# Kernel optimization log

Measured on AMD Instinct MI355X. Metric: run time of the kernel, lower is better.

## Reference

```python
import jax, jax.numpy as jnp
import numpy as np

DIM = 768
NUM_HEADS = 12
HEAD_DIM = DIM // NUM_HEADS
ROPE_BASE = 10000.0


def _rope_angles(height, width, head_dim, base):
    # 2D RoPE: first half of head_dim rotates with the row (y) position,
    # second half with the column (x) position.
    half = head_dim // 2            # dims per spatial axis
    quarter = half // 2             # rotation pair count per axis
    inv_freq = 1.0 / (base ** (jnp.arange(0, half, 2, dtype=jnp.float32) / half))  # [quarter]
    ys = jnp.arange(height, dtype=jnp.float32)
    xs = jnp.arange(width, dtype=jnp.float32)
    ang_y = ys[:, None] * inv_freq  # [H, quarter]
    ang_x = xs[:, None] * inv_freq  # [W, quarter]
    ay = jnp.broadcast_to(ang_y[:, None, :], (height, width, quarter)).reshape(height * width, quarter)
    ax = jnp.broadcast_to(ang_x[None, :, :], (height, width, quarter)).reshape(height * width, quarter)
    return ay, ax


def _rotate(t, ang):
    # t: [B, nh, N, half]; ang: [N, quarter]. Interleaved pair rotation.
    c, s = jnp.cos(ang), jnp.sin(ang)
    t1, t2 = t[..., 0::2], t[..., 1::2]
    r1 = t1 * c - t2 * s
    r2 = t1 * s + t2 * c
    return jnp.stack([r1, r2], axis=-1).reshape(t.shape)


def apply_2d_rope(t, height, width, base):
    # t: [B, nh, N, head_dim]
    hd = t.shape[-1]
    half = hd // 2
    ay, ax = _rope_angles(height, width, hd, base)
    return jnp.concatenate([_rotate(t[..., :half], ay), _rotate(t[..., half:], ax)], axis=-1)


def setup_inputs() -> dict:
    key = jax.random.key(0)
    ks = jax.random.split(key, 5)
    B, N = 16, 32 * 32
    x = jax.random.normal(ks[0], (B, N, DIM), dtype=jnp.float32)
    qkv_w = jax.random.normal(ks[1], (3 * DIM, DIM), dtype=jnp.float32) * (1.0 / np.sqrt(DIM))
    qkv_b = jnp.zeros((3 * DIM,), dtype=jnp.float32)
    proj_w = jax.random.normal(ks[2], (DIM, DIM), dtype=jnp.float32) * (1.0 / np.sqrt(DIM))
    proj_b = jnp.zeros((DIM,), dtype=jnp.float32)
    return {"x": x, "qkv_w": qkv_w, "qkv_b": qkv_b, "proj_w": proj_w,
            "proj_b": proj_b, "height": 32, "width": 32}


def reference(x, qkv_w, qkv_b, proj_w, proj_b, height, width):
    B, N, C = x.shape
    scale = 1.0 / np.sqrt(HEAD_DIM)
    qkv = x @ qkv_w.T + qkv_b                      # [B, N, 3*C]
    qkv = qkv.reshape(B, N, 3, NUM_HEADS, HEAD_DIM).transpose(2, 0, 3, 1, 4)
    q, k, v = qkv[0], qkv[1], qkv[2]               # [B, nh, N, hd]
    q = apply_2d_rope(q, height, width, ROPE_BASE)
    k = apply_2d_rope(k, height, width, ROPE_BASE)
    attn = jnp.einsum('bhnd,bhmd->bhnm', q, k) * scale
    attn = jax.nn.softmax(attn, axis=-1)
    out = jnp.einsum('bhnm,bhmd->bhnd', attn, v)   # [B, nh, N, hd]
    out = out.transpose(0, 2, 1, 3).reshape(B, N, C)
    return out @ proj_w.T + proj_b
```

## Files before the change

### kernel.cpp

```cpp
#include <hip/hip_runtime.h>
#include <hip/hip_bf16.h>

typedef _Float16 f16;
typedef _Float16 half8 __attribute__((ext_vector_type(8)));
typedef _Float16 half4 __attribute__((ext_vector_type(4)));
typedef float f32x4 __attribute__((ext_vector_type(4)));
typedef unsigned short u16;
typedef unsigned int u32;

#define AS_GLOBAL __attribute__((address_space(1)))
#define AS_LDS    __attribute__((address_space(3)))

static __device__ __forceinline__ f32x4 mfma_k32(half8 a, half8 b, f32x4 c) {
  return __builtin_amdgcn_mfma_f32_16x16x32_f16(a, b, c, 0, 0, 0);
}

static __device__ __forceinline__ void glds16(const void* g, void* l) {
  __builtin_amdgcn_global_load_lds((const AS_GLOBAL u32*)(unsigned long long)g,
                                   (AS_LDS u32*)l, 16, 0, 0);
}

__global__ __launch_bounds__(256) void cvt_kernel(const float* __restrict__ src,
                                                  f16* __restrict__ dst, int n) {
  long i = ((long)blockIdx.x * 256 + threadIdx.x) * 8;
  if (i + 8 <= n) {
    const float4 a = *(const float4*)(src + i);
    const float4 b = *(const float4*)(src + i + 4);
    union { uint4 v; f16 h[8]; } o;
    o.h[0] = (f16)a.x; o.h[1] = (f16)a.y; o.h[2] = (f16)a.z; o.h[3] = (f16)a.w;
    o.h[4] = (f16)b.x; o.h[5] = (f16)b.y; o.h[6] = (f16)b.z; o.h[7] = (f16)b.w;
    *(uint4*)(dst + i) = o.v;
  }
}

static __device__ __forceinline__ void gemm128p(const f16* __restrict__ A, const f16* __restrict__ B,
                                                const int K, const long m0, const long n0,
                                                f16* As, f16* Bs, f32x4 acc[4][4]) {
  const int tid = threadIdx.x;
  const int lane = tid & 63, w = tid >> 6;
  const int l15 = lane & 15, qd = lane >> 4;
  const int wr = w >> 1, wc = w & 1;
  const int srow = w * 16 + (lane >> 2);
  const int sg   = ((lane & 3) ^ ((lane >> 3) & 3)) * 8;
  const f16* gA0 = A + (m0 + srow) * (long)K + sg;
  const f16* gA1 = gA0 + 64 * (long)K;
  const f16* gB0 = B + (n0 + srow) * (long)K + sg;
  const f16* gB1 = gB0 + 64 * (long)K;
  f16* lA = As + w * 512;
  f16* lB = Bs + w * 512;
  const int rg   = (qd ^ ((l15 >> 1) & 3)) * 8;
  const int arow = (wr * 64 + l15) * 32;
  const int brow = (wc * 64 + l15) * 32;
  const int nT = K >> 5;

#define STAGE(t) { const long ko = (long)(t) * 32;                         \
    f16* dA = lA + ((t) % 3) * 4096; f16* dB = lB + ((t) % 3) * 4096;      \
    glds16(gA0 + ko, dA); glds16(gA1 + ko, dA + 2048);                     \
    glds16(gB0 + ko, dB); glds16(gB1 + ko, dB + 2048); }

  STAGE(0); STAGE(1);
  asm volatile("s_waitcnt vmcnt(4)" ::: "memory");
  __builtin_amdgcn_sched_barrier(0);
  __builtin_amdgcn_s_barrier();
  __builtin_amdgcn_sched_barrier(0);
#pragma unroll
  for (int t = 0; t < nT; ++t) {
    if (t + 2 < nT) STAGE(t + 2);
    const f16* cA = As + (t % 3) * 4096;
    const f16* cB = Bs + (t % 3) * 4096;
    half8 a0[2], a1[2], b0[2], b1[2];
    a0[0] = *(const half8*)(cA + arow + rg);
    a0[1] = *(const half8*)(cA + arow + 512 + rg);
    b0[0] = *(const half8*)(cB + brow + rg);
    b0[1] = *(const half8*)(cB + brow + 512 + rg);
    __builtin_amdgcn_s_setprio(1);
    acc[0][0] = mfma_k32(a0[0], b0[0], acc[0][0]);
    acc[0][1] = mfma_k32(a0[0], b0[1], acc[0][1]);
    acc[1][0] = mfma_k32(a0[1], b0[0], acc[1][0]);
    acc[1][1] = mfma_k32(a0[1], b0[1], acc[1][1]);
    __builtin_amdgcn_s_setprio(0);
    b1[0] = *(const half8*)(cB + brow + 1024 + rg);
    b1[1] = *(const half8*)(cB + brow + 1536 + rg);
    __builtin_amdgcn_s_setprio(1);
    acc[0][2] = mfma_k32(a0[0], b1[0], acc[0][2]);
    acc[0][3] = mfma_k32(a0[0], b1[1], acc[0][3]);
    acc[1][2] = mfma_k32(a0[1], b1[0], acc[1][2]);
    acc[1][3] = mfma_k32(a0[1], b1[1], acc[1][3]);
    __builtin_amdgcn_s_setprio(0);
    a1[0] = *(const half8*)(cA + arow + 1024 + rg);
    a1[1] = *(const half8*)(cA + arow + 1536 + rg);
    __builtin_amdgcn_s_setprio(1);
    acc[2][2] = mfma_k32(a1[0], b1[0], acc[2][2]);
    acc[2][3] = mfma_k32(a1[0], b1[1], acc[2][3]);
    acc[3][2] = mfma_k32(a1[1], b1[0], acc[3][2]);
    acc[3][3] = mfma_k32(a1[1], b1[1], acc[3][3]);
    acc[2][0] = mfma_k32(a1[0], b0[0], acc[2][0]);
    acc[2][1] = mfma_k32(a1[0], b0[1], acc[2][1]);
    acc[3][0] = mfma_k32(a1[1], b0[0], acc[3][0]);
    acc[3][1] = mfma_k32(a1[1], b0[1], acc[3][1]);
    __builtin_amdgcn_s_setprio(0);
    if (t < nT - 1) {
      if (t == nT - 2) { asm volatile("s_waitcnt vmcnt(0)" ::: "memory"); }
      else             { asm volatile("s_waitcnt vmcnt(4)" ::: "memory"); }
      __builtin_amdgcn_sched_barrier(0);
      __builtin_amdgcn_s_barrier();
      __builtin_amdgcn_sched_barrier(0);
    }
  }
#undef STAGE
}

__global__ __launch_bounds__(256) void qkv_kernel(const f16* __restrict__ X, const f16* __restrict__ W,
                                                  const float* __restrict__ bias,
                                                  f16* __restrict__ Qf, f16* __restrict__ Kf,
                                                  f16* __restrict__ Vf) {
  __shared__ __align__(16) f16 As[12288];
  __shared__ __align__(16) f16 Bs[12288];
  f32x4 acc[4][4];
#pragma unroll
  for (int i = 0; i < 4; ++i)
#pragma unroll
    for (int j = 0; j < 4; ++j) acc[i][j] = (f32x4){0.f, 0.f, 0.f, 0.f};
  const long m0 = (long)blockIdx.x * 128;
  const long n0 = (long)blockIdx.y * 128;
  gemm128p(X, W, 768, m0, n0, As, Bs, acc);

  const int tid = threadIdx.x, lane = tid & 63, w = tid >> 6;
  const int l15 = lane & 15, qd = lane >> 4;
  const int wr = w >> 1, wc = w & 1;
  const int bb = (int)(m0 >> 10);
  const int slot = (int)(n0 >> 6) + wc;
  const int which = slot / 12, h = slot % 12;
  f16* dst0 = (which == 0) ? Qf : (which == 1) ? Kf : Vf;
  f16* dstbh = dst0 + ((long)(bb * 12 + h)) * 1024 * 64;
  const bool doRope = (which != 2);
  const bool isQ = (which == 0);
  const bool odd = (l15 & 1);
#pragma unroll
  for (int j = 0; j < 4; ++j) {
    const int d = 16 * j + l15;
    const int p = d >> 1;
    const float fr = exp2f(-0.8304820237218405f * (float)(p & 15));
    const bool useY = (p < 16);
    const float bv = bias[n0 + 64 * wc + d];
#pragma unroll
    for (int i = 0; i < 4; ++i) {
      const int nbase = (int)(m0 & 1023) + 64 * wr + 16 * i + qd * 4;
#pragma unroll
      for (int r = 0; r < 4; ++r) {
        const int n = nbase + r;
        float v = acc[i][j][r] + bv;
        if (doRope) {
          const float pv = __shfl_xor(v, 1, 64);
          const float pos = useY ? (float)(n >> 5) : (float)(n & 31);
          float sn, cn;
          __sincosf(pos * fr, &sn, &cn);
          float res = odd ? (pv * sn + v * cn) : (v * cn - pv * sn);
          if (isQ) res *= 0.18033688011112042f;
          v = res;
        }
        dstbh[(long)n * 64 + d] = (f16)v;
      }
    }
  }
}

__global__ __launch_bounds__(256) void attn_kernel(const f16* __restrict__ Qf, const f16* __restrict__ Kf,
                                                   const f16* __restrict__ Vf, f16* __restrict__ Aout) {
  const int lin = (int)blockIdx.x + ((int)blockIdx.y << 3);
  const int xcd = lin & 7, idx = lin >> 3;
  const int bh = xcd * 24 + (idx >> 3);
  const int qt = idx & 7;
  const int b = bh / 12, h = bh % 12;
  const int tid = threadIdx.x;
  const int lane = tid & 63, w = tid >> 6;
  const int l15 = lane & 15, qd = lane >> 4;

  __shared__ __align__(16) f16 Ks[64][72];
  __shared__ __align__(16) f16 Vts[64][72];
  __shared__ float wsum[128];

  const f16* Qg = Qf + ((long)bh * 1024 + qt * 128) * 64;
  const f16* Kg = Kf + (long)bh * 1024 * 64;
  const f16* Vg = Vf + (long)bh * 1024 * 64;

  half8 qb[2][2];
#pragma unroll
  for (int g = 0; g < 2; ++g)
#pragma unroll
    for (int dc = 0; dc < 2; ++dc)
      qb[g][dc] = *(const half8*)(Qg + (w * 32 + g * 16 + l15) * 64 + dc * 32 + qd * 8);

  float lsum[2] = {0.f, 0.f};
  f32x4 O[2][4];
#pragma unroll
  for (int g = 0; g < 2; ++g)
#pragma unroll
    for (int nt = 0; nt < 4; ++nt) O[g][nt] = (f32x4){0.f, 0.f, 0.f, 0.f};

  const int srow = tid >> 2, sch = (tid & 3) * 16;
  const f16* kgb = Kg + (long)srow * 64 + sch;
  const int sk0 = (tid & 31) * 2, scd = tid >> 5;
  const f16* vgb = Vg + (long)sk0 * 64 + scd * 8;
  uint4 kr0, kr1, vr0, vr1;

  kr0 = *(const uint4*)(kgb);
  kr1 = *(const uint4*)(kgb + 8);
  vr0 = *(const uint4*)(vgb);
  vr1 = *(const uint4*)(vgb + 64);

  for (int kt = 0; kt < 16; ++kt) {
    *(uint4*)(&Ks[srow][sch])     = kr0;
    *(uint4*)(&Ks[srow][sch + 8]) = kr1;
    {
      union { uint4 u; f16 hh[8]; } ua, ub;
      ua.u = vr0; ub.u = vr1;
#pragma unroll
      for (int i2 = 0; i2 < 8; ++i2) {
        union { u32 u; f16 hh[2]; } t2;
        t2.hh[0] = ua.hh[i2]; t2.hh[1] = ub.hh[i2];
        *(u32*)(&Vts[scd * 8 + i2][sk0]) = t2.u;
      }
    }
    __syncthreads();

    if (kt < 15) {
      const f16* kp = kgb + (kt + 1) * 4096;
      kr0 = *(const uint4*)(kp);
      kr1 = *(const uint4*)(kp + 8);
      const f16* vp = vgb + (kt + 1) * 4096;
      vr0 = *(const uint4*)(vp);
      vr1 = *(const uint4*)(vp + 64);
    }

    f32x4 S[2][4];
#pragma unroll
    for (int kb = 0; kb < 4; ++kb) {
      const half8 ka0 = *(const half8*)(&Ks[kb * 16 + l15][qd * 8]);
      const half8 ka1 = *(const half8*)(&Ks[kb * 16 + l15][32 + qd * 8]);
#pragma unroll
      for (int g = 0; g < 2; ++g) {
        f32x4 z = (f32x4){0.f, 0.f, 0.f, 0.f};
        z = mfma_k32(ka0, qb[g][0], z);
        z = mfma_k32(ka1, qb[g][1], z);
        S[g][kb] = z;
      }
    }

    half8 pa8[2][2];
#pragma unroll
    for (int g = 0; g < 2; ++g)
#pragma unroll
      for (int c = 0; c < 2; ++c) {
        const f32x4 s0 = S[g][2 * c], s1 = S[g][2 * c + 1];
        const float p0 = __builtin_amdgcn_exp2f(s0[0]);
        const float p1 = __builtin_amdgcn_exp2f(s0[1]);
        const float p2 = __builtin_amdgcn_exp2f(s0[2]);
        const float p3 = __builtin_amdgcn_exp2f(s0[3]);
        const float p4 = __builtin_amdgcn_exp2f(s1[0]);
        const float p5 = __builtin_amdgcn_exp2f(s1[1]);
        const float p6 = __builtin_amdgcn_exp2f(s1[2]);
        const float p7 = __builtin_amdgcn_exp2f(s1[3]);
        lsum[g] += ((p0 + p1) + (p2 + p3)) + ((p4 + p5) + (p6 + p7));
        half8 pk;
        pk[0] = (f16)p0; pk[1] = (f16)p1; pk[2] = (f16)p2; pk[3] = (f16)p3;
        pk[4] = (f16)p4; pk[5] = (f16)p5; pk[6] = (f16)p6; pk[7] = (f16)p7;
        pa8[g][c] = pk;
      }

#pragma unroll
    for (int nt = 0; nt < 4; ++nt) {
      half8 vv[2];
#pragma unroll
      for (int c = 0; c < 2; ++c) {
        const half4 v0 = *(const half4*)(&Vts[nt * 16 + l15][c * 32 + qd * 4]);
        const half4 v1 = *(const half4*)(&Vts[nt * 16 + l15][c * 32 + 16 + qd * 4]);
        vv[c] = __builtin_shufflevector(v0, v1, 0, 1, 2, 3, 4, 5, 6, 7);
      }
#pragma unroll
      for (int g = 0; g < 2; ++g) {
        O[g][nt] = mfma_k32(pa8[g][0], vv[0], O[g][nt]);
        O[g][nt] = mfma_k32(pa8[g][1], vv[1], O[g][nt]);
      }
    }
    __syncthreads();
  }

#pragma unroll
  for (int g = 0; g < 2; ++g) {
    float s = lsum[g];
    s += __shfl_xor(s, 16, 64);
    s += __shfl_xor(s, 32, 64);
    if (lane < 16) wsum[w * 32 + g * 16 + lane] = s;
  }
  __syncthreads();
  float inv[2][4];
#pragma unroll
  for (int g = 0; g < 2; ++g)
#pragma unroll
    for (int r = 0; r < 4; ++r)
      inv[g][r] = 1.f / wsum[w * 32 + g * 16 + qd * 4 + r];
#pragma unroll
  for (int g = 0; g < 2; ++g)
#pragma unroll
    for (int r = 0; r < 4; ++r) {
      const int n = qt * 128 + w * 32 + g * 16 + qd * 4 + r;
      f16* dst = Aout + ((long)b * 1024 + n) * 768 + h * 64;
#pragma unroll
      for (int nt = 0; nt < 4; ++nt)
        dst[nt * 16 + l15] = (f16)(O[g][nt][r] * inv[g][r]);
    }
}

__global__ __launch_bounds__(256) void proj_kernel(const f16* __restrict__ A, const f16* __restrict__ W,
                                                   const float* __restrict__ bias, float* __restrict__ out) {
  __shared__ __align__(16) f16 As[12288];
  __shared__ __align__(16) f16 Bs[12288];
  f32x4 acc[4][4];
#pragma unroll
  for (int i = 0; i < 4; ++i)
#pragma unroll
    for (int j = 0; j < 4; ++j) acc[i][j] = (f32x4){0.f, 0.f, 0.f, 0.f};
  const long m0 = (long)blockIdx.x * 128;
  const long n0 = (long)blockIdx.y * 128;
  gemm128p(A, W, 768, m0, n0, As, Bs, acc);

  const int tid = threadIdx.x, lane = tid & 63, w = tid >> 6;
  const int l15 = lane & 15, qd = lane >> 4;
  const int wr = w >> 1, wc = w & 1;
#pragma unroll
  for (int j = 0; j < 4; ++j) {
    const int col = (int)n0 + 64 * wc + 16 * j + l15;
    const float bv = bias[col];
#pragma unroll
    for (int i = 0; i < 4; ++i) {
      const long m = m0 + 64 * wr + 16 * i + qd * 4;
#pragma unroll
      for (int r = 0; r < 4; ++r)
        out[(m + r) * 768 + col] = acc[i][j][r] + bv;
    }
  }
}

extern "C" void kernel_launch(void* const* d_in, const int* in_sizes, int n_in,
                              void* d_out, int out_size, void* d_ws, size_t ws_size,
                              hipStream_t stream) {
  const float* x_f    = (const float*)d_in[0];
  const float* qkvw_f = (const float*)d_in[1];
  const float* qkvb_f = (const float*)d_in[2];
  const float* projw_f= (const float*)d_in[3];
  const float* projb_f= (const float*)d_in[4];

  char* ws = (char*)d_ws;
  f16* xh   = (f16*)(ws + 0);
  f16* wqh  = (f16*)(ws + 25165824);
  f16* wph  = (f16*)(ws + 28704768);
  f16* Qf   = (f16*)(ws + 29884416);
  f16* Kf   = (f16*)(ws + 55050240);
  f16* Vf   = (f16*)(ws + 80216064);
  f16* Aout = (f16*)(ws + 0);

  cvt_kernel<<<6144, 256, 0, stream>>>(x_f, xh, 12582912);
  cvt_kernel<<<864, 256, 0, stream>>>(qkvw_f, wqh, 1769472);
  cvt_kernel<<<288, 256, 0, stream>>>(projw_f, wph, 589824);
  qkv_kernel<<<dim3(128, 18), 256, 0, stream>>>(xh, wqh, qkvb_f, Qf, Kf, Vf);
  attn_kernel<<<dim3(8, 192), 256, 0, stream>>>(Qf, Kf, Vf, Aout);
  proj_kernel<<<dim3(128, 6), 256, 0, stream>>>(Aout, wph, projb_f, (float*)d_out);
}
```

Before: 303.4 us.

## Double-buffer K/V tiles in attention and merge the three conversion launches

The attention kernel now keeps two LDS buffers for the K and V tiles. The next tile is written into the idle buffer while the current one is consumed, so each iteration needs one barrier instead of two, and global prefetch runs two tiles ahead. The three fp32-to-fp16 conversion launches are merged into a single kernel that picks its source by block index, saving two launch gaps. The cost is double the LDS for K and V, which may lower attention occupancy.

```diff
diff --git a/kernel.cpp b/kernel.cpp
--- a/kernel.cpp
+++ b/kernel.cpp
@@ -20,17 +20,24 @@
                                    (AS_LDS u32*)l, 16, 0, 0);
 }
 
-__global__ __launch_bounds__(256) void cvt_kernel(const float* __restrict__ src,
-                                                  f16* __restrict__ dst, int n) {
-  long i = ((long)blockIdx.x * 256 + threadIdx.x) * 8;
-  if (i + 8 <= n) {
-    const float4 a = *(const float4*)(src + i);
-    const float4 b = *(const float4*)(src + i + 4);
-    union { uint4 v; f16 h[8]; } o;
-    o.h[0] = (f16)a.x; o.h[1] = (f16)a.y; o.h[2] = (f16)a.z; o.h[3] = (f16)a.w;
-    o.h[4] = (f16)b.x; o.h[5] = (f16)b.y; o.h[6] = (f16)b.z; o.h[7] = (f16)b.w;
-    *(uint4*)(dst + i) = o.v;
-  }
+__global__ __launch_bounds__(256) void cvt_all_kernel(const float* __restrict__ x,
+                                                      const float* __restrict__ w1,
+                                                      const float* __restrict__ w2,
+                                                      f16* __restrict__ xo,
+                                                      f16* __restrict__ w1o,
+                                                      f16* __restrict__ w2o) {
+  const int bx = blockIdx.x;
+  const float* src; f16* dst; long base;
+  if (bx < 6144)      { src = x;  dst = xo;  base = (long)bx * 2048; }
+  else if (bx < 7008) { src = w1; dst = w1o; base = (long)(bx - 6144) * 2048; }
+  else                { src = w2; dst = w2o; base = (long)(bx - 7008) * 2048; }
+  const long i = base + (long)threadIdx.x * 8;
+  const float4 a = *(const float4*)(src + i);
+  const float4 b = *(const float4*)(src + i + 4);
+  union { uint4 v; f16 h[8]; } o;
+  o.h[0] = (f16)a.x; o.h[1] = (f16)a.y; o.h[2] = (f16)a.z; o.h[3] = (f16)a.w;
+  o.h[4] = (f16)b.x; o.h[5] = (f16)b.y; o.h[6] = (f16)b.z; o.h[7] = (f16)b.w;
+  *(uint4*)(dst + i) = o.v;
 }
 
 static __device__ __forceinline__ void gemm128p(const f16* __restrict__ A, const f16* __restrict__ B,
@@ -176,8 +183,8 @@
   const int lane = tid & 63, w = tid >> 6;
   const int l15 = lane & 15, qd = lane >> 4;
 
-  __shared__ __align__(16) f16 Ks[64][72];
-  __shared__ __align__(16) f16 Vts[64][72];
+  __shared__ __align__(16) f16 Ks[2][64][72];
+  __shared__ __align__(16) f16 Vts[2][64][72];
   __shared__ float wsum[128];
 
   const f16* Qg = Qf + ((long)bh * 1024 + qt * 128) * 64;
@@ -204,31 +211,38 @@
   const f16* vgb = Vg + (long)sk0 * 64 + scd * 8;
   uint4 kr0, kr1, vr0, vr1;
 
+  auto writeKV = [&](int buf) {
+    *(uint4*)(&Ks[buf][srow][sch])     = kr0;
+    *(uint4*)(&Ks[buf][srow][sch + 8]) = kr1;
+    union { uint4 u; f16 hh[8]; } ua, ub;
+    ua.u = vr0; ub.u = vr1;
+#pragma unroll
+    for (int i2 = 0; i2 < 8; ++i2) {
+      union { u32 u; f16 hh[2]; } t2;
+      t2.hh[0] = ua.hh[i2]; t2.hh[1] = ub.hh[i2];
+      *(u32*)(&Vts[buf][scd * 8 + i2][sk0]) = t2.u;
+    }
+  };
+
   kr0 = *(const uint4*)(kgb);
   kr1 = *(const uint4*)(kgb + 8);
   vr0 = *(const uint4*)(vgb);
   vr1 = *(const uint4*)(vgb + 64);
+  writeKV(0);
+  kr0 = *(const uint4*)(kgb + 4096);
+  kr1 = *(const uint4*)(kgb + 4096 + 8);
+  vr0 = *(const uint4*)(vgb + 4096);
+  vr1 = *(const uint4*)(vgb + 4096 + 64);
+  __syncthreads();
 
   for (int kt = 0; kt < 16; ++kt) {
-    *(uint4*)(&Ks[srow][sch])     = kr0;
-    *(uint4*)(&Ks[srow][sch + 8]) = kr1;
-    {
-      union { uint4 u; f16 hh[8]; } ua, ub;
-      ua.u = vr0; ub.u = vr1;
-#pragma unroll
-      for (int i2 = 0; i2 < 8; ++i2) {
-        union { u32 u; f16 hh[2]; } t2;
-        t2.hh[0] = ua.hh[i2]; t2.hh[1] = ub.hh[i2];
-        *(u32*)(&Vts[scd * 8 + i2][sk0]) = t2.u;
-      }
-    }
-    __syncthreads();
-
-    if (kt < 15) {
-      const f16* kp = kgb + (kt + 1) * 4096;
+    const int cur = kt & 1;
+    if (kt < 15) writeKV(cur ^ 1);
+    if (kt < 14) {
+      const f16* kp = kgb + (kt + 2) * 4096;
       kr0 = *(const uint4*)(kp);
       kr1 = *(const uint4*)(kp + 8);
-      const f16* vp = vgb + (kt + 1) * 4096;
+      const f16* vp = vgb + (kt + 2) * 4096;
       vr0 = *(const uint4*)(vp);
       vr1 = *(const uint4*)(vp + 64);
     }
@@ -236,8 +250,8 @@
     f32x4 S[2][4];
 #pragma unroll
     for (int kb = 0; kb < 4; ++kb) {
-      const half8 ka0 = *(const half8*)(&Ks[kb * 16 + l15][qd * 8]);
-      const half8 ka1 = *(const half8*)(&Ks[kb * 16 + l15][32 + qd * 8]);
+      const half8 ka0 = *(const half8*)(&Ks[cur][kb * 16 + l15][qd * 8]);
+      const half8 ka1 = *(const half8*)(&Ks[cur][kb * 16 + l15][32 + qd * 8]);
 #pragma unroll
       for (int g = 0; g < 2; ++g) {
         f32x4 z = (f32x4){0.f, 0.f, 0.f, 0.f};
@@ -273,8 +287,8 @@
       half8 vv[2];
 #pragma unroll
       for (int c = 0; c < 2; ++c) {
-        const half4 v0 = *(const half4*)(&Vts[nt * 16 + l15][c * 32 + qd * 4]);
-        const half4 v1 = *(const half4*)(&Vts[nt * 16 + l15][c * 32 + 16 + qd * 4]);
+        const half4 v0 = *(const half4*)(&Vts[cur][nt * 16 + l15][c * 32 + qd * 4]);
+        const half4 v1 = *(const half4*)(&Vts[cur][nt * 16 + l15][c * 32 + 16 + qd * 4]);
         vv[c] = __builtin_shufflevector(v0, v1, 0, 1, 2, 3, 4, 5, 6, 7);
       }
 #pragma unroll
@@ -360,9 +374,7 @@
   f16* Vf   = (f16*)(ws + 80216064);
   f16* Aout = (f16*)(ws + 0);
 
-  cvt_kernel<<<6144, 256, 0, stream>>>(x_f, xh, 12582912);
-  cvt_kernel<<<864, 256, 0, stream>>>(qkvw_f, wqh, 1769472);
-  cvt_kernel<<<288, 256, 0, stream>>>(projw_f, wph, 589824);
+  cvt_all_kernel<<<7296, 256, 0, stream>>>(x_f, qkvw_f, projw_f, xh, wqh, wph);
   qkv_kernel<<<dim3(128, 18), 256, 0, stream>>>(xh, wqh, qkvb_f, Qf, Kf, Vf);
   attn_kernel<<<dim3(8, 192), 256, 0, stream>>>(Qf, Kf, Vf, Aout);
   proj_kernel<<<dim3(128, 6), 256, 0, stream>>>(Aout, wph, projb_f, (float*)d_out);
```

Measured after the change: 297.4 us. About the same (-1.9%).
